# Kernel optimization log

Measured on AMD Instinct MI355X. Metric: run time of the kernel, lower is better.

## Reference

```python
import jax, jax.numpy as jnp
import numpy as np

N_NODES = 50000
BN_EPS = 1e-5


def gcn_conv(x, W, b, src, dst, ew):
    # x: [N, Fin], W: [Fin, Fout]; PyG GCNConv with self loops and edge weights
    xw = x @ W
    loop = jnp.arange(N_NODES)
    s = jnp.concatenate([src, loop])
    d = jnp.concatenate([dst, loop])
    w = jnp.concatenate([ew, jnp.ones((N_NODES,), ew.dtype)])
    deg = jax.ops.segment_sum(w, d, num_segments=N_NODES)
    dinv = jnp.where(deg > 0, jax.lax.rsqrt(deg), 0.0)
    norm = dinv[s] * w * dinv[d]                      # [E+N]
    msg = norm[:, None] * xw[s]                       # [E+N, Fout]
    out = jax.ops.segment_sum(msg, d, num_segments=N_NODES)
    return out + b


def batch_norm(x, gamma, beta):
    mu = jnp.mean(x, axis=0)
    var = jnp.mean(jnp.square(x - mu), axis=0)
    return gamma * (x - mu) * jax.lax.rsqrt(var + BN_EPS) + beta


def setup_inputs() -> dict:
    key = jax.random.key(0)
    ks = jax.random.split(key, 6)
    F_IN, H, C, E = 128, 128, 40, 800000
    x = jax.random.normal(ks[0], (N_NODES, F_IN), jnp.float32)
    edge_index = jax.random.randint(ks[1], (2, E), 0, N_NODES, jnp.int64)
    edge_weight = jax.random.uniform(ks[2], (E,), jnp.float32)
    W1 = jax.random.normal(ks[3], (F_IN, H), jnp.float32) / np.sqrt(F_IN)
    W2 = jax.random.normal(ks[4], (H, H), jnp.float32) / np.sqrt(H)
    W3 = jax.random.normal(ks[5], (H, C), jnp.float32) / np.sqrt(H)
    return {
        "x": x, "edge_index": edge_index, "edge_weight": edge_weight,
        "W1": W1, "b1": jnp.zeros((H,), jnp.float32),
        "gamma1": jnp.ones((H,), jnp.float32), "beta1": jnp.zeros((H,), jnp.float32),
        "W2": W2, "b2": jnp.zeros((H,), jnp.float32),
        "gamma2": jnp.ones((H,), jnp.float32), "beta2": jnp.zeros((H,), jnp.float32),
        "W3": W3, "b3": jnp.zeros((C,), jnp.float32),
    }


def reference(x, edge_index, edge_weight, W1, b1, gamma1, beta1,
              W2, b2, gamma2, beta2, W3, b3):
    src, dst = edge_index[0], edge_index[1]
    h = gcn_conv(x, W1, b1, src, dst, edge_weight)
    h = jax.nn.relu(batch_norm(h, gamma1, beta1))   # dropout = identity (eval)
    h = gcn_conv(h, W2, b2, src, dst, edge_weight)
    h = jax.nn.relu(batch_norm(h, gamma2, beta2))
    h = gcn_conv(h, W3, b3, src, dst, edge_weight)
    return jax.nn.log_softmax(h, axis=-1)
```

## Files before the change

### kernel.cpp

```cpp
#include <hip/hip_runtime.h>
#include <cstdint>
#include <cstddef>

#define N_NODES 50000
#define BN_EPS 1e-5f
#define NPB 256
#define NB ((N_NODES + NPB - 1) / NPB)
#define EPB 2048
#define BN_BLOCKS 128

typedef unsigned int uint32;
typedef unsigned short ushort;

typedef short bf16x8 __attribute__((ext_vector_type(8)));
typedef float f32x4 __attribute__((ext_vector_type(4)));


__device__ inline ushort bf16rn(float f) {
  unsigned int u = __float_as_uint(f);
  u += 0x7fffu + ((u >> 16) & 1u);
  return (ushort)(u >> 16);
}
__device__ inline float unbf(uint32 u) { return __uint_as_float(u << 16); }
__device__ inline float lo16(uint32 u) { return __uint_as_float(u << 16); }
__device__ inline float hi16(uint32 u) { return __uint_as_float(u & 0xffff0000u); }
__device__ inline uint32 pack2(float a, float b) {
  return (uint32)bf16rn(a) | ((uint32)bf16rn(b) << 16);
}


__global__ __launch_bounds__(256) void k_cvtW_all(const float* __restrict__ W1,
    const float* __restrict__ W2, const float* __restrict__ W3,
    ushort* __restrict__ Wt1, ushort* __restrict__ Wt2, ushort* __restrict__ Wt3) {
  int gid = blockIdx.x * 256 + threadIdx.x;
  if (gid < 16384) {
    int c = gid >> 7, k = gid & 127;
    Wt1[c * 128 + k] = bf16rn(W1[(size_t)k * 128 + c]);
  } else if (gid < 32768) {
    int g = gid - 16384, c = g >> 7, k = g & 127;
    Wt2[c * 128 + k] = bf16rn(W2[(size_t)k * 128 + c]);
  } else if (gid < 37888) {
    int g = gid - 32768, c = g >> 7, k = g & 127;
    Wt3[c * 128 + k] = bf16rn(W3[(size_t)k * 40 + c]);
  }
}


__global__ __launch_bounds__(256) void k_ehist(const int* __restrict__ dst, int E,
    int* __restrict__ histB, int* __restrict__ hists) {
  __shared__ int h[NB];
  for (int i = threadIdx.x; i < NB; i += 256) h[i] = 0;
  __syncthreads();
  int base = blockIdx.x * EPB;
  for (int i = threadIdx.x; i < EPB; i += 256) {
    int e = base + i;
    if (e < E) atomicAdd(&h[dst[e] >> 8], 1);
  }
  __syncthreads();
  for (int i = threadIdx.x; i < NB; i += 256) {
    int v = h[i];
    hists[blockIdx.x * NB + i] = v;
    if (v) atomicAdd(&histB[i], v);
  }
}

__global__ void k_prefix(const int* __restrict__ histB, int E,
                         int* __restrict__ rbase, int* __restrict__ cbase,
                         int* __restrict__ start) {
  if (threadIdx.x == 0 && blockIdx.x == 0) {
    int r = 0, c = 0;
    for (int b = 0; b < NB; ++b) {
      int npb = (b == NB - 1) ? (N_NODES - b * NPB) : NPB;
      rbase[b] = r; cbase[b] = c;
      r += histB[b]; c += histB[b] + npb;
    }
    rbase[NB] = r;
    start[N_NODES] = c;
  }
}

__global__ __launch_bounds__(256) void k_binA(const int* __restrict__ src,
    const int* __restrict__ dst, const float* __restrict__ ew, int E,
    const int* __restrict__ rbase, const int* __restrict__ hists,
    int* __restrict__ gcur, uint2* __restrict__ bins) {
  __shared__ int gb[NB], cur[NB];
  for (int i = threadIdx.x; i < NB; i += 256) {
    int hv = hists[blockIdx.x * NB + i];
    cur[i] = 0;
    gb[i] = hv ? (rbase[i] + atomicAdd(&gcur[i], hv)) : 0;
  }
  __syncthreads();
  int base = blockIdx.x * EPB;
  for (int i = threadIdx.x; i < EPB; i += 256) {
    int e = base + i;
    if (e < E) {
      int d = dst[e];
      int g = d >> 8;
      int p = gb[g] + atomicAdd(&cur[g], 1);
      bins[p] = make_uint2((uint32)src[e] | ((uint32)(d & 255) << 16),
                           __float_as_uint(ew[e]));
    }
  }
}

__global__ __launch_bounds__(256) void k_binB(const uint2* __restrict__ bins,
    const int* __restrict__ rbase, const int* __restrict__ cbase,
    int* __restrict__ start, float* __restrict__ dinv, uint32* __restrict__ csr) {
  __shared__ int h[256], cur[256], ofs[256], sc[256];
  __shared__ float deg[256];
  int tid = threadIdx.x;
  int b = blockIdx.x;
  int node0 = b << 8;
  int npb = min(NPB, N_NODES - node0);
  h[tid] = 0; deg[tid] = 1.0f;
  __syncthreads();
  int r0 = rbase[b], r1 = rbase[b + 1];
  for (int i = r0 + tid; i < r1; i += 256) {
    uint2 rec = bins[i];
    int dl = (rec.x >> 16) & 255;
    atomicAdd(&h[dl], 1);
    atomicAdd(&deg[dl], __uint_as_float(rec.y));
  }
  __syncthreads();
  int v = (tid < npb) ? 1 + h[tid] : 0;
  sc[tid] = v;
  __syncthreads();
  for (int off = 1; off < 256; off <<= 1) {
    int a = (tid >= off) ? sc[tid - off] : 0;
    __syncthreads();
    sc[tid] += a;
    __syncthreads();
  }
  int cb = cbase[b];
  if (tid < npb) {
    int segBase = cb + sc[tid] - v;
    int node = node0 + tid;
    start[node] = segBase;
    csr[segBase] = (0x3F80u << 16) | (uint32)node;
    dinv[node] = rsqrtf(deg[tid]);
    ofs[tid] = segBase + 1;
    cur[tid] = 0;
  }
  __syncthreads();
  for (int i = r0 + tid; i < r1; i += 256) {
    uint2 rec = bins[i];
    int dl = (rec.x >> 16) & 255;
    int p = ofs[dl] + atomicAdd(&cur[dl], 1);
    csr[p] = ((uint32)bf16rn(__uint_as_float(rec.y)) << 16) | (rec.x & 0xffff);
  }
}

__global__ __launch_bounds__(256) void k_wnorm(uint32* __restrict__ csr,
    const int* __restrict__ start, const float* __restrict__ dinv) {
  int lane = threadIdx.x & 15;
  int node = blockIdx.x * 16 + (threadIdx.x >> 4);
  if (node >= N_NODES) return;
  float di = dinv[node];
  int e0 = start[node], e1 = start[node + 1];
  for (int e = e0 + lane; e < e1; e += 16) {
    uint32 c = csr[e];
    int s = c & 0xffff;
    float w = unbf(c >> 16) * dinv[s] * di;
    csr[e] = ((uint32)bf16rn(w) << 16) | (uint32)s;
  }
}


template <int BNT, typename XT>
__global__ __launch_bounds__(256) void k_mfma(const XT* __restrict__ X,
    const ushort* __restrict__ Wt, const float* __restrict__ ssb,
    ushort* __restrict__ out16, int Fout) {
  __shared__ ushort Xs[64][136];
  __shared__ ushort Bs[BNT * 16][136];
  int tid = threadIdx.x;
  int r0 = blockIdx.x * 64;

  for (int idx = tid; idx < BNT * 16 * 16; idx += 256) {
    int col = idx >> 4;
    int kk = (idx & 15) * 8;
    uint4 v = make_uint4(0, 0, 0, 0);
    if (col < Fout)
      v = *reinterpret_cast<const uint4*>(&Wt[(size_t)col * 128 + kk]);
    *reinterpret_cast<uint4*>(&Bs[col][kk]) = v;
  }

  if (sizeof(XT) == 4) {
    const float* Xf = reinterpret_cast<const float*>(X);
    for (int idx = tid; idx < 2048; idx += 256) {
      int row = idx >> 5;
      int kk = (idx & 31) * 4;
      int gr = r0 + row;
      float4 v = make_float4(0.f, 0.f, 0.f, 0.f);
      if (gr < N_NODES)
        v = *reinterpret_cast<const float4*>(&Xf[(size_t)gr * 128 + kk]);
      ushort4 o;
      o.x = bf16rn(v.x); o.y = bf16rn(v.y); o.z = bf16rn(v.z); o.w = bf16rn(v.w);
      *reinterpret_cast<ushort4*>(&Xs[row][kk]) = o;
    }
  } else {
    const ushort* X16 = reinterpret_cast<const ushort*>(X);
    for (int idx = tid; idx < 1024; idx += 256) {
      int row = idx >> 4;
      int kk = (idx & 15) * 8;
      int gr = r0 + row;
      uint4 v = make_uint4(0, 0, 0, 0);
      if (gr < N_NODES)
        v = *reinterpret_cast<const uint4*>(&X16[(size_t)gr * 128 + kk]);
      if (ssb) {
        float f[8] = { lo16(v.x), hi16(v.x), lo16(v.y), hi16(v.y),
                       lo16(v.z), hi16(v.z), lo16(v.w), hi16(v.w) };
        float4 sc0 = *reinterpret_cast<const float4*>(&ssb[kk]);
        float4 sc1 = *reinterpret_cast<const float4*>(&ssb[kk + 4]);
        float4 sh0 = *reinterpret_cast<const float4*>(&ssb[128 + kk]);
        float4 sh1 = *reinterpret_cast<const float4*>(&ssb[128 + kk + 4]);
        f[0] = fmaxf(0.f, f[0] * sc0.x + sh0.x);
        f[1] = fmaxf(0.f, f[1] * sc0.y + sh0.y);
        f[2] = fmaxf(0.f, f[2] * sc0.z + sh0.z);
        f[3] = fmaxf(0.f, f[3] * sc0.w + sh0.w);
        f[4] = fmaxf(0.f, f[4] * sc1.x + sh1.x);
        f[5] = fmaxf(0.f, f[5] * sc1.y + sh1.y);
        f[6] = fmaxf(0.f, f[6] * sc1.z + sh1.z);
        f[7] = fmaxf(0.f, f[7] * sc1.w + sh1.w);
        v.x = pack2(f[0], f[1]); v.y = pack2(f[2], f[3]);
        v.z = pack2(f[4], f[5]); v.w = pack2(f[6], f[7]);
      }
      *reinterpret_cast<uint4*>(&Xs[row][kk]) = v;
    }
  }
  __syncthreads();

  int lane = tid & 63, wav = tid >> 6;
  int lrow = lane & 15, lk = (lane >> 4) * 8;
  f32x4 acc[BNT];
  #pragma unroll
  for (int ct = 0; ct < BNT; ++ct) acc[ct] = (f32x4){0.f, 0.f, 0.f, 0.f};

  #pragma unroll
  for (int kc = 0; kc < 4; ++kc) {
    int k0 = kc * 32 + lk;
    bf16x8 a = *reinterpret_cast<const bf16x8*>(&Xs[wav * 16 + lrow][k0]);
    #pragma unroll
    for (int ct = 0; ct < BNT; ++ct) {
      bf16x8 b = *reinterpret_cast<const bf16x8*>(&Bs[ct * 16 + lrow][k0]);
      acc[ct] = __builtin_amdgcn_mfma_f32_16x16x32_bf16(a, b, acc[ct], 0, 0, 0);
    }
  }

  int orow = wav * 16 + (lane >> 4) * 4;
  #pragma unroll
  for (int ct = 0; ct < BNT; ++ct) {
    int gc = ct * 16 + lrow;
    if (gc >= Fout) continue;
    #pragma unroll
    for (int i = 0; i < 4; ++i) {
      int gr = r0 + orow + i;
      if (gr < N_NODES) out16[(size_t)gr * Fout + gc] = bf16rn(acc[ct][i]);
    }
  }
}


__global__ __launch_bounds__(256) void k_agg128c(const ushort* __restrict__ xw,
    const float* __restrict__ bias, const int* __restrict__ start,
    const uint32* __restrict__ csr, ushort* __restrict__ out16) {
  int lane = threadIdx.x & 63;
  int node = blockIdx.x * 4 + (threadIdx.x >> 6);
  if (node >= N_NODES) return;
  int sub = lane >> 4;
  int fl  = lane & 15;
  const uint4* rows = (const uint4*)xw;
  float acc[8] = {};
  int e0 = start[node], e1 = start[node + 1];
  int e = e0 + sub;
  for (; e + 4 < e1; e += 8) {
    uint32 c0 = csr[e], c1 = csr[e + 4];
    uint4 v0 = rows[(size_t)(c0 & 0xffff) * 16 + fl];
    uint4 v1 = rows[(size_t)(c1 & 0xffff) * 16 + fl];
    float w0 = unbf(c0 >> 16), w1 = unbf(c1 >> 16);
    acc[0] += w0 * lo16(v0.x) + w1 * lo16(v1.x);
    acc[1] += w0 * hi16(v0.x) + w1 * hi16(v1.x);
    acc[2] += w0 * lo16(v0.y) + w1 * lo16(v1.y);
    acc[3] += w0 * hi16(v0.y) + w1 * hi16(v1.y);
    acc[4] += w0 * lo16(v0.z) + w1 * lo16(v1.z);
    acc[5] += w0 * hi16(v0.z) + w1 * hi16(v1.z);
    acc[6] += w0 * lo16(v0.w) + w1 * lo16(v1.w);
    acc[7] += w0 * hi16(v0.w) + w1 * hi16(v1.w);
  }
  if (e < e1) {
    uint32 c = csr[e];
    float w = unbf(c >> 16);
    uint4 v = rows[(size_t)(c & 0xffff) * 16 + fl];
    acc[0] += w * lo16(v.x); acc[1] += w * hi16(v.x);
    acc[2] += w * lo16(v.y); acc[3] += w * hi16(v.y);
    acc[4] += w * lo16(v.z); acc[5] += w * hi16(v.z);
    acc[6] += w * lo16(v.w); acc[7] += w * hi16(v.w);
  }
  #pragma unroll
  for (int k = 0; k < 8; ++k) acc[k] += __shfl_xor(acc[k], 16);
  #pragma unroll
  for (int k = 0; k < 8; ++k) acc[k] += __shfl_xor(acc[k], 32);
  if (sub == 0) {
    float4 b0 = ((const float4*)bias)[fl * 2];
    float4 b1 = ((const float4*)bias)[fl * 2 + 1];
    acc[0] += b0.x; acc[1] += b0.y; acc[2] += b0.z; acc[3] += b0.w;
    acc[4] += b1.x; acc[5] += b1.y; acc[6] += b1.z; acc[7] += b1.w;
    uint4 o;
    o.x = pack2(acc[0], acc[1]);
    o.y = pack2(acc[2], acc[3]);
    o.z = pack2(acc[4], acc[5]);
    o.w = pack2(acc[6], acc[7]);
    ((uint4*)out16)[(size_t)node * 16 + fl] = o;
  }
}


__global__ __launch_bounds__(256) void k_agg40lsm(const ushort* __restrict__ xw,
    const float* __restrict__ bias, const int* __restrict__ start,
    const uint32* __restrict__ csr, float* __restrict__ out) {
  int lane = threadIdx.x & 63;
  int node = blockIdx.x * 4 + (threadIdx.x >> 6);
  if (node >= N_NODES) return;
  int sub = lane >> 4;
  int fl  = lane & 15;
  bool active = fl < 10;
  int flc = active ? fl : 0;
  const uint2* rows = (const uint2*)xw;
  float acc[4] = {};
  int e0 = start[node], e1 = start[node + 1];
  for (int e = e0 + sub; e < e1; e += 4) {
    uint32 c = csr[e];
    float w = unbf(c >> 16);
    int s = c & 0xffff;
    uint2 v = rows[(size_t)s * 10 + flc];
    if (active) {
      acc[0] += w * lo16(v.x); acc[1] += w * hi16(v.x);
      acc[2] += w * lo16(v.y); acc[3] += w * hi16(v.y);
    }
  }
  #pragma unroll
  for (int k = 0; k < 4; ++k) acc[k] += __shfl_xor(acc[k], 16);
  #pragma unroll
  for (int k = 0; k < 4; ++k) acc[k] += __shfl_xor(acc[k], 32);
  if (sub == 0) {
    float m = -1e30f, es = 0.f;
    if (active) {
      float4 b = ((const float4*)bias)[fl];
      acc[0] += b.x; acc[1] += b.y; acc[2] += b.z; acc[3] += b.w;
      m = fmaxf(fmaxf(acc[0], acc[1]), fmaxf(acc[2], acc[3]));
    }
    #pragma unroll
    for (int off = 8; off >= 1; off >>= 1) m = fmaxf(m, __shfl_xor(m, off, 16));
    if (active)
      es = expf(acc[0] - m) + expf(acc[1] - m) + expf(acc[2] - m) + expf(acc[3] - m);
    #pragma unroll
    for (int off = 8; off >= 1; off >>= 1) es += __shfl_xor(es, off, 16);
    if (active) {
      float lse = m + logf(es);
      float4 o = make_float4(acc[0] - lse, acc[1] - lse, acc[2] - lse, acc[3] - lse);
      *reinterpret_cast<float4*>(&out[(size_t)node * 40 + fl * 4]) = o;
    }
  }
}


__global__ __launch_bounds__(256) void k_bnstats1(const ushort* __restrict__ x,
    float* __restrict__ partials) {
  int fl = threadIdx.x & 15;
  int rg = threadIdx.x >> 4;
  float s[8] = {}, q[8] = {};
  const uint4* xv = (const uint4*)x;
  for (int row = blockIdx.x * 16 + rg; row < N_NODES; row += BN_BLOCKS * 16) {
    uint4 v = xv[(size_t)row * 16 + fl];
    float f0 = lo16(v.x), f1 = hi16(v.x), f2 = lo16(v.y), f3 = hi16(v.y);
    float f4 = lo16(v.z), f5 = hi16(v.z), f6 = lo16(v.w), f7 = hi16(v.w);
    s[0] += f0; q[0] += f0 * f0; s[1] += f1; q[1] += f1 * f1;
    s[2] += f2; q[2] += f2 * f2; s[3] += f3; q[3] += f3 * f3;
    s[4] += f4; q[4] += f4 * f4; s[5] += f5; q[5] += f5 * f5;
    s[6] += f6; q[6] += f6 * f6; s[7] += f7; q[7] += f7 * f7;
  }
  __shared__ float ls[256][8];
  __shared__ float lq[256][8];
  #pragma unroll
  for (int j = 0; j < 8; ++j) { ls[threadIdx.x][j] = s[j]; lq[threadIdx.x][j] = q[j]; }
  __syncthreads();
  for (int step = 8; step >= 1; step >>= 1) {
    if (rg < step) {
      #pragma unroll
      for (int j = 0; j < 8; ++j) {
        ls[rg * 16 + fl][j] += ls[(rg + step) * 16 + fl][j];
        lq[rg * 16 + fl][j] += lq[(rg + step) * 16 + fl][j];
      }
    }
    __syncthreads();
  }
  if (rg == 0) {
    #pragma unroll
    for (int j = 0; j < 8; ++j) {
      partials[(size_t)blockIdx.x * 256 + fl * 8 + j] = ls[fl][j];
      partials[(size_t)blockIdx.x * 256 + 128 + fl * 8 + j] = lq[fl][j];
    }
  }
}


__global__ __launch_bounds__(256) void k_bnred(const float* __restrict__ partials,
    const float* __restrict__ gamma, const float* __restrict__ beta,
    float* __restrict__ ssb) {
  int tid = threadIdx.x;
  float s = 0.f;
  for (int b = 0; b < BN_BLOCKS; ++b) s += partials[(size_t)b * 256 + tid];
  __shared__ float st[256];
  st[tid] = s;
  __syncthreads();
  if (tid < 128) {
    float inv_n = 1.0f / (float)N_NODES;
    float mu = st[tid] * inv_n;
    float var = st[128 + tid] * inv_n - mu * mu;
    if (var < 0.f) var = 0.f;
    float sc = gamma[tid] * rsqrtf(var + BN_EPS);
    ssb[tid] = sc;
    ssb[128 + tid] = beta[tid] - mu * sc;
  }
}


extern "C" void kernel_launch(void* const* d_in, const int* in_sizes, int n_in,
                              void* d_out, int out_size, void* d_ws, size_t ws_size,
                              hipStream_t stream) {
  const float* x   = (const float*)d_in[0];
  const int*   ei  = (const int*)d_in[1];
  const float* ew  = (const float*)d_in[2];
  const float* W1  = (const float*)d_in[3];
  const float* b1  = (const float*)d_in[4];
  const float* g1  = (const float*)d_in[5];
  const float* be1 = (const float*)d_in[6];
  const float* W2  = (const float*)d_in[7];
  const float* b2  = (const float*)d_in[8];
  const float* g2  = (const float*)d_in[9];
  const float* be2 = (const float*)d_in[10];
  const float* W3  = (const float*)d_in[11];
  const float* b3  = (const float*)d_in[12];
  float* out = (float*)d_out;
  int E = in_sizes[2];
  const int* src = ei;
  const int* dst = ei + E;
  int nblkA = (E + EPB - 1) / EPB;

  char* p = (char*)d_ws;
  auto alloc = [&](size_t bytes) {
    char* r = p; p += (bytes + 255) & ~(size_t)255; return r;
  };
  int*    histB  = (int*)   alloc((size_t)(NB + 1) * 4);
  int*    gcur   = (int*)   alloc((size_t)NB * 4);
  size_t zspan = (size_t)((char*)gcur + (size_t)NB * 4 - (char*)histB);
  int*    rbase  = (int*)   alloc((size_t)(NB + 1) * 4);
  int*    cbase  = (int*)   alloc((size_t)NB * 4);
  int*    hists  = (int*)   alloc((size_t)nblkA * NB * 4);
  int*    startA = (int*)   alloc((size_t)(N_NODES + 1) * 4);
  float*  dinv   = (float*) alloc((size_t)N_NODES * 4);
  uint2*  bins   = (uint2*) alloc((size_t)E * 8);
  uint32* csr    = (uint32*)alloc((size_t)(E + N_NODES) * 4);
  float*  parts  = (float*) alloc((size_t)BN_BLOCKS * 256 * 4);
  float*  ssb1   = (float*) alloc(256 * 4);
  float*  ssb2   = (float*) alloc(256 * 4);
  ushort* Wt1    = (ushort*)alloc((size_t)128 * 128 * 2);
  ushort* Wt2    = (ushort*)alloc((size_t)128 * 128 * 2);
  ushort* Wt3    = (ushort*)alloc((size_t)40 * 128 * 2);
  ushort* xw16   = (ushort*)alloc((size_t)N_NODES * 128 * 2);
  ushort* buf16  = (ushort*)alloc((size_t)N_NODES * 128 * 2);

  hipMemsetAsync(histB, 0, zspan, stream);
  k_cvtW_all<<<149, 256, 0, stream>>>(W1, W2, W3, Wt1, Wt2, Wt3);
  k_ehist<<<nblkA, 256, 0, stream>>>(dst, E, histB, hists);
  k_prefix<<<1, 64, 0, stream>>>(histB, E, rbase, cbase, startA);
  k_binA<<<nblkA, 256, 0, stream>>>(src, dst, ew, E, rbase, hists, gcur, bins);
  k_binB<<<NB, 256, 0, stream>>>(bins, rbase, cbase, startA, dinv, csr);
  k_wnorm<<<(N_NODES + 15) / 16, 256, 0, stream>>>(csr, startA, dinv);

  int gemmGrid = (N_NODES + 63) / 64;
  int aggGrid = (N_NODES + 3) / 4;

  k_mfma<8, float><<<gemmGrid, 256, 0, stream>>>(x, Wt1, nullptr, xw16, 128);
  k_agg128c<<<aggGrid, 256, 0, stream>>>(xw16, b1, startA, csr, buf16);
  k_bnstats1<<<BN_BLOCKS, 256, 0, stream>>>(buf16, parts);
  k_bnred<<<1, 256, 0, stream>>>(parts, g1, be1, ssb1);

  k_mfma<8, ushort><<<gemmGrid, 256, 0, stream>>>(buf16, Wt2, ssb1, xw16, 128);
  k_agg128c<<<aggGrid, 256, 0, stream>>>(xw16, b2, startA, csr, buf16);
  k_bnstats1<<<BN_BLOCKS, 256, 0, stream>>>(buf16, parts);
  k_bnred<<<1, 256, 0, stream>>>(parts, g2, be2, ssb2);

  k_mfma<3, ushort><<<gemmGrid, 256, 0, stream>>>(buf16, Wt3, ssb2, xw16, 40);
  k_agg40lsm<<<aggGrid, 256, 0, stream>>>(xw16, b3, startA, csr, out);
}
```

Before: 235.7 us.

## Fold prefix and BN-reduce kernels into last-block epilogues; unroll aggregation loops

Removes the separate single-block k_prefix and k_bnred launches. Their work now runs in the last block of k_ehist and k_bnstats1, which is detected with an atomic done counter and thread fences. The counters are zeroed by the existing memset. The 128-feature aggregation loop is also unrolled from 2 to 4 edges per step, and the 40-feature loop from 1 to 2, so more independent gathers are in flight. The aim is to cut launch gaps and hide memory latency, at the cost of extra registers and a serial tail in the last block.

New measurement: 237.8 us. No clear change (+0.9%).

```diff
diff --git a/kernel.cpp b/kernel.cpp
--- a/kernel.cpp
+++ b/kernel.cpp
@@ -47,7 +47,8 @@
 
 
 __global__ __launch_bounds__(256) void k_ehist(const int* __restrict__ dst, int E,
-    int* __restrict__ histB, int* __restrict__ hists) {
+    int* __restrict__ histB, int* __restrict__ hists, int* __restrict__ done,
+    int* __restrict__ rbase, int* __restrict__ cbase, int* __restrict__ start) {
   __shared__ int h[NB];
   for (int i = threadIdx.x; i < NB; i += 256) h[i] = 0;
   __syncthreads();
@@ -62,20 +63,20 @@
     hists[blockIdx.x * NB + i] = v;
     if (v) atomicAdd(&histB[i], v);
   }
-}
-
-__global__ void k_prefix(const int* __restrict__ histB, int E,
-                         int* __restrict__ rbase, int* __restrict__ cbase,
-                         int* __restrict__ start) {
-  if (threadIdx.x == 0 && blockIdx.x == 0) {
-    int r = 0, c = 0;
-    for (int b = 0; b < NB; ++b) {
-      int npb = (b == NB - 1) ? (N_NODES - b * NPB) : NPB;
-      rbase[b] = r; cbase[b] = c;
-      r += histB[b]; c += histB[b] + npb;
-    }
-    rbase[NB] = r;
-    start[N_NODES] = c;
+  if (threadIdx.x == 0) {
+    __threadfence();
+    int old = atomicAdd(done, 1);
+    if (old == gridDim.x - 1) {
+      __threadfence();
+      int r = 0, c = 0;
+      for (int b = 0; b < NB; ++b) {
+        int npb = (b == NB - 1) ? (N_NODES - b * NPB) : NPB;
+        rbase[b] = r; cbase[b] = c;
+        r += histB[b]; c += histB[b] + npb;
+      }
+      rbase[NB] = r;
+      start[N_NODES] = c;
+    }
   }
 }
 
@@ -272,21 +273,24 @@
   float acc[8] = {};
   int e0 = start[node], e1 = start[node + 1];
   int e = e0 + sub;
-  for (; e + 4 < e1; e += 8) {
-    uint32 c0 = csr[e], c1 = csr[e + 4];
+  for (; e + 12 < e1; e += 16) {
+    uint32 c0 = csr[e], c1 = csr[e + 4], c2 = csr[e + 8], c3 = csr[e + 12];
     uint4 v0 = rows[(size_t)(c0 & 0xffff) * 16 + fl];
     uint4 v1 = rows[(size_t)(c1 & 0xffff) * 16 + fl];
+    uint4 v2 = rows[(size_t)(c2 & 0xffff) * 16 + fl];
+    uint4 v3 = rows[(size_t)(c3 & 0xffff) * 16 + fl];
     float w0 = unbf(c0 >> 16), w1 = unbf(c1 >> 16);
-    acc[0] += w0 * lo16(v0.x) + w1 * lo16(v1.x);
-    acc[1] += w0 * hi16(v0.x) + w1 * hi16(v1.x);
-    acc[2] += w0 * lo16(v0.y) + w1 * lo16(v1.y);
-    acc[3] += w0 * hi16(v0.y) + w1 * hi16(v1.y);
-    acc[4] += w0 * lo16(v0.z) + w1 * lo16(v1.z);
-    acc[5] += w0 * hi16(v0.z) + w1 * hi16(v1.z);
-    acc[6] += w0 * lo16(v0.w) + w1 * lo16(v1.w);
-    acc[7] += w0 * hi16(v0.w) + w1 * hi16(v1.w);
-  }
-  if (e < e1) {
+    float w2 = unbf(c2 >> 16), w3 = unbf(c3 >> 16);
+    acc[0] += w0 * lo16(v0.x) + w1 * lo16(v1.x) + w2 * lo16(v2.x) + w3 * lo16(v3.x);
+    acc[1] += w0 * hi16(v0.x) + w1 * hi16(v1.x) + w2 * hi16(v2.x) + w3 * hi16(v3.x);
+    acc[2] += w0 * lo16(v0.y) + w1 * lo16(v1.y) + w2 * lo16(v2.y) + w3 * lo16(v3.y);
+    acc[3] += w0 * hi16(v0.y) + w1 * hi16(v1.y) + w2 * hi16(v2.y) + w3 * hi16(v3.y);
+    acc[4] += w0 * lo16(v0.z) + w1 * lo16(v1.z) + w2 * lo16(v2.z) + w3 * lo16(v3.z);
+    acc[5] += w0 * hi16(v0.z) + w1 * hi16(v1.z) + w2 * hi16(v2.z) + w3 * hi16(v3.z);
+    acc[6] += w0 * lo16(v0.w) + w1 * lo16(v1.w) + w2 * lo16(v2.w) + w3 * lo16(v3.w);
+    acc[7] += w0 * hi16(v0.w) + w1 * hi16(v1.w) + w2 * hi16(v2.w) + w3 * hi16(v3.w);
+  }
+  for (; e < e1; e += 4) {
     uint32 c = csr[e];
     float w = unbf(c >> 16);
     uint4 v = rows[(size_t)(c & 0xffff) * 16 + fl];
@@ -327,11 +331,23 @@
   const uint2* rows = (const uint2*)xw;
   float acc[4] = {};
   int e0 = start[node], e1 = start[node + 1];
-  for (int e = e0 + sub; e < e1; e += 4) {
+  int e = e0 + sub;
+  for (; e + 4 < e1; e += 8) {
+    uint32 c0 = csr[e], c1 = csr[e + 4];
+    uint2 v0 = rows[(size_t)(c0 & 0xffff) * 10 + flc];
+    uint2 v1 = rows[(size_t)(c1 & 0xffff) * 10 + flc];
+    float w0 = unbf(c0 >> 16), w1 = unbf(c1 >> 16);
+    if (active) {
+      acc[0] += w0 * lo16(v0.x) + w1 * lo16(v1.x);
+      acc[1] += w0 * hi16(v0.x) + w1 * hi16(v1.x);
+      acc[2] += w0 * lo16(v0.y) + w1 * lo16(v1.y);
+      acc[3] += w0 * hi16(v0.y) + w1 * hi16(v1.y);
+    }
+  }
+  if (e < e1) {
     uint32 c = csr[e];
     float w = unbf(c >> 16);
-    int s = c & 0xffff;
-    uint2 v = rows[(size_t)s * 10 + flc];
+    uint2 v = rows[(size_t)(c & 0xffff) * 10 + flc];
     if (active) {
       acc[0] += w * lo16(v.x); acc[1] += w * hi16(v.x);
       acc[2] += w * lo16(v.y); acc[3] += w * hi16(v.y);
@@ -364,9 +380,12 @@
 
 
 __global__ __launch_bounds__(256) void k_bnstats1(const ushort* __restrict__ x,
-    float* __restrict__ partials) {
-  int fl = threadIdx.x & 15;
-  int rg = threadIdx.x >> 4;
+    float* __restrict__ partials, int* __restrict__ done,
+    const float* __restrict__ gamma, const float* __restrict__ beta,
+    float* __restrict__ ssb) {
+  int tid = threadIdx.x;
+  int fl = tid & 15;
+  int rg = tid >> 4;
   float s[8] = {}, q[8] = {};
   const uint4* xv = (const uint4*)x;
   for (int row = blockIdx.x * 16 + rg; row < N_NODES; row += BN_BLOCKS * 16) {
@@ -381,7 +400,7 @@
   __shared__ float ls[256][8];
   __shared__ float lq[256][8];
   #pragma unroll
-  for (int j = 0; j < 8; ++j) { ls[threadIdx.x][j] = s[j]; lq[threadIdx.x][j] = q[j]; }
+  for (int j = 0; j < 8; ++j) { ls[tid][j] = s[j]; lq[tid][j] = q[j]; }
   __syncthreads();
   for (int step = 8; step >= 1; step >>= 1) {
     if (rg < step) {
@@ -400,26 +419,29 @@
       partials[(size_t)blockIdx.x * 256 + 128 + fl * 8 + j] = lq[fl][j];
     }
   }
-}
-
-
-__global__ __launch_bounds__(256) void k_bnred(const float* __restrict__ partials,
-    const float* __restrict__ gamma, const float* __restrict__ beta,
-    float* __restrict__ ssb) {
-  int tid = threadIdx.x;
-  float s = 0.f;
-  for (int b = 0; b < BN_BLOCKS; ++b) s += partials[(size_t)b * 256 + tid];
-  __shared__ float st[256];
-  st[tid] = s;
-  __syncthreads();
-  if (tid < 128) {
-    float inv_n = 1.0f / (float)N_NODES;
-    float mu = st[tid] * inv_n;
-    float var = st[128 + tid] * inv_n - mu * mu;
-    if (var < 0.f) var = 0.f;
-    float sc = gamma[tid] * rsqrtf(var + BN_EPS);
-    ssb[tid] = sc;
-    ssb[128 + tid] = beta[tid] - mu * sc;
+  __shared__ int isLast;
+  __syncthreads();
+  if (tid == 0) {
+    __threadfence();
+    isLast = (atomicAdd(done, 1) == BN_BLOCKS - 1) ? 1 : 0;
+  }
+  __syncthreads();
+  if (isLast) {
+    __threadfence();
+    float acc = 0.f;
+    for (int b = 0; b < BN_BLOCKS; ++b) acc += partials[(size_t)b * 256 + tid];
+    __shared__ float st[256];
+    st[tid] = acc;
+    __syncthreads();
+    if (tid < 128) {
+      float inv_n = 1.0f / (float)N_NODES;
+      float mu = st[tid] * inv_n;
+      float var = st[128 + tid] * inv_n - mu * mu;
+      if (var < 0.f) var = 0.f;
+      float sc = gamma[tid] * rsqrtf(var + BN_EPS);
+      ssb[tid] = sc;
+      ssb[128 + tid] = beta[tid] - mu * sc;
+    }
   }
 }
 
@@ -452,7 +474,10 @@
   };
   int*    histB  = (int*)   alloc((size_t)(NB + 1) * 4);
   int*    gcur   = (int*)   alloc((size_t)NB * 4);
-  size_t zspan = (size_t)((char*)gcur + (size_t)NB * 4 - (char*)histB);
+  int*    doneE  = (int*)   alloc(4);
+  int*    doneB1 = (int*)   alloc(4);
+  int*    doneB2 = (int*)   alloc(4);
+  size_t zspan = (size_t)((char*)doneB2 + 4 - (char*)histB);
   int*    rbase  = (int*)   alloc((size_t)(NB + 1) * 4);
   int*    cbase  = (int*)   alloc((size_t)NB * 4);
   int*    hists  = (int*)   alloc((size_t)nblkA * NB * 4);
@@ -471,8 +496,7 @@
 
   hipMemsetAsync(histB, 0, zspan, stream);
   k_cvtW_all<<<149, 256, 0, stream>>>(W1, W2, W3, Wt1, Wt2, Wt3);
-  k_ehist<<<nblkA, 256, 0, stream>>>(dst, E, histB, hists);
-  k_prefix<<<1, 64, 0, stream>>>(histB, E, rbase, cbase, startA);
+  k_ehist<<<nblkA, 256, 0, stream>>>(dst, E, histB, hists, doneE, rbase, cbase, startA);
   k_binA<<<nblkA, 256, 0, stream>>>(src, dst, ew, E, rbase, hists, gcur, bins);
   k_binB<<<NB, 256, 0, stream>>>(bins, rbase, cbase, startA, dinv, csr);
   k_wnorm<<<(N_NODES + 15) / 16, 256, 0, stream>>>(csr, startA, dinv);
@@ -482,13 +506,11 @@
 
   k_mfma<8, float><<<gemmGrid, 256, 0, stream>>>(x, Wt1, nullptr, xw16, 128);
   k_agg128c<<<aggGrid, 256, 0, stream>>>(xw16, b1, startA, csr, buf16);
-  k_bnstats1<<<BN_BLOCKS, 256, 0, stream>>>(buf16, parts);
-  k_bnred<<<1, 256, 0, stream>>>(parts, g1, be1, ssb1);
+  k_bnstats1<<<BN_BLOCKS, 256, 0, stream>>>(buf16, parts, doneB1, g1, be1, ssb1);
 
   k_mfma<8, ushort><<<gemmGrid, 256, 0, stream>>>(buf16, Wt2, ssb1, xw16, 128);
   k_agg128c<<<aggGrid, 256, 0, stream>>>(xw16, b2, startA, csr, buf16);
-  k_bnstats1<<<BN_BLOCKS, 256, 0, stream>>>(buf16, parts);
-  k_bnred<<<1, 256, 0, stream>>>(parts, g2, be2, ssb2);
+  k_bnstats1<<<BN_BLOCKS, 256, 0, stream>>>(buf16, parts, doneB2, g2, be2, ssb2);
 
   k_mfma<3, ushort><<<gemmGrid, 256, 0, stream>>>(buf16, Wt3, ssb2, xw16, 40);
   k_agg40lsm<<<aggGrid, 256, 0, stream>>>(xw16, b3, startA, csr, out);
```
